# Optimization experiments

Hardware: AMD Instinct MI355X
Metric: run time of the kernel (lower is better)

## Reference

```python
import jax, jax.numpy as jnp
import numpy as np

N_LEAVES = 8192   # perfect binary tree, depth 13
SEQ = 4096        # sequenceSize
EMB = 100         # embedSize
NCLS = 2          # numClasses


def setup_inputs() -> dict:
    key = jax.random.key(0)
    k = jax.random.split(key, 7)
    return {
        "leaf_seqs": jax.random.normal(k[0], (N_LEAVES, SEQ), dtype=jnp.float32),
        # torch nn.Linear stores weight as [out, in]; y = x @ W.T + b
        "We": jax.random.normal(k[1], (EMB, SEQ), dtype=jnp.float32) / np.sqrt(SEQ).astype(np.float32),
        "be": jax.random.normal(k[2], (EMB,), dtype=jnp.float32) * 0.01,
        "W": jax.random.normal(k[3], (EMB, 2 * EMB), dtype=jnp.float32) / np.sqrt(2 * EMB).astype(np.float32),
        "b": jax.random.normal(k[4], (EMB,), dtype=jnp.float32) * 0.01,
        "Wp": jax.random.normal(k[5], (NCLS, EMB), dtype=jnp.float32) / np.sqrt(EMB).astype(np.float32),
        "bp": jax.random.normal(k[6], (NCLS,), dtype=jnp.float32) * 0.01,
    }


def reference(leaf_seqs, We, be, W, b, Wp, bp):
    # Level-order (tree-batched) evaluation of the recursive RNN over a
    # perfect binary tree. Leaves: relu(embedding(seq)); internal nodes:
    # relu(W @ cat(left, right)); root: projection -> class logits.
    h = jax.nn.relu(leaf_seqs @ We.T + be)              # [n_leaves, emb]
    depth = int(np.log2(N_LEAVES))
    for _ in range(depth):                               # fixed small loop over levels
        # adjacent siblings: reshape gives cat((left, right), dim=1) per pair
        pairs = h.reshape(h.shape[0] // 2, 2 * h.shape[1])  # [n/2, 2*emb]
        h = jax.nn.relu(pairs @ W.T + b)                 # [n/2, emb]
    logits = h @ Wp.T + bp                               # [1, numClasses]
    return logits
```

## Files before the change

### kernel.cpp

```cpp
#include <hip/hip_runtime.h>


typedef _Float16 half_t;
typedef __attribute__((ext_vector_type(8))) _Float16 half8;
typedef __attribute__((ext_vector_type(4))) float floatx4;

__global__ __launch_bounds__(256) void bprep(const float* __restrict__ We,
                                             half_t* __restrict__ Bf) {
  int t = blockIdx.x * 256 + threadIdx.x;
  int lane = t & 63;
  int c = (t >> 6) & 7;
  int ks = t >> 9;
  int q = lane >> 4, m = lane & 15;
  int n = c * 16 + m;
  int k0 = ks * 32 + q * 8;

  half8 hv, lv;
#pragma unroll
  for (int j = 0; j < 8; ++j) {
    float w = (n < 100) ? We[(size_t)n * 4096 + k0 + j] : 0.f;
    half_t hh = (half_t)w;
    hv[j] = hh;
    lv[j] = (half_t)(w - (float)hh);
  }
  size_t fhi = (size_t)(ks * 16 + c * 2 + 0) * 64 + lane;
  size_t flo = (size_t)(ks * 16 + c * 2 + 1) * 64 + lane;
  *(half8*)(Bf + fhi * 8) = hv;
  *(half8*)(Bf + flo * 8) = lv;
}

__global__ __launch_bounds__(512, 1) void leaf_mfma(const float* __restrict__ A,
                                                    const half8* __restrict__ Bf,
                                                    const float* __restrict__ be,
                                                    float* __restrict__ h0) {
  __shared__ float red[4 * 32 * 128];
  const int tid = threadIdx.x;
  const int lane = tid & 63;
  const int wave = tid >> 6;
  const int q = lane >> 4, m = lane & 15;
  const int r0 = blockIdx.x * 32;

  floatx4 acc[2][8];
#pragma unroll
  for (int t = 0; t < 2; ++t)
#pragma unroll
    for (int c = 0; c < 8; ++c) acc[t][c] = (floatx4){0.f, 0.f, 0.f, 0.f};

  const float* a0 = A + (size_t)(r0 + m) * 4096 + wave * 512 + q * 8;
  const float* a1 = a0 + (size_t)16 * 4096;
  const half8* bw = Bf + (size_t)wave * 256 * 64 + lane;

  floatx4 acur[4], anxt[4];
  acur[0] = *(const floatx4*)(a0);
  acur[1] = *(const floatx4*)(a0 + 4);
  acur[2] = *(const floatx4*)(a1);
  acur[3] = *(const floatx4*)(a1 + 4);

  for (int s = 0; s < 16; ++s) {
    if (s < 15) {
      const float* p0 = a0 + (s + 1) * 32;
      const float* p1 = a1 + (s + 1) * 32;
      anxt[0] = *(const floatx4*)(p0);
      anxt[1] = *(const floatx4*)(p0 + 4);
      anxt[2] = *(const floatx4*)(p1);
      anxt[3] = *(const floatx4*)(p1 + 4);
    }
    half8 ahi[2], alo[2];
#pragma unroll
    for (int t = 0; t < 2; ++t) {
#pragma unroll
      for (int j = 0; j < 8; ++j) {
        float v = acur[2 * t + (j >> 2)][j & 3];
        half_t hh = (half_t)v;
        ahi[t][j] = hh;
        alo[t][j] = (half_t)(v - (float)hh);
      }
    }
    const half8* bs = bw + s * 1024;
#pragma unroll
    for (int c = 0; c < 8; ++c) {
      half8 bhi = bs[c * 128];
      half8 blo = bs[c * 128 + 64];
      acc[0][c] = __builtin_amdgcn_mfma_f32_16x16x32_f16(ahi[0], bhi, acc[0][c], 0, 0, 0);
      acc[1][c] = __builtin_amdgcn_mfma_f32_16x16x32_f16(ahi[1], bhi, acc[1][c], 0, 0, 0);
      acc[0][c] = __builtin_amdgcn_mfma_f32_16x16x32_f16(alo[0], bhi, acc[0][c], 0, 0, 0);
      acc[1][c] = __builtin_amdgcn_mfma_f32_16x16x32_f16(alo[1], bhi, acc[1][c], 0, 0, 0);
      acc[0][c] = __builtin_amdgcn_mfma_f32_16x16x32_f16(ahi[0], blo, acc[0][c], 0, 0, 0);
      acc[1][c] = __builtin_amdgcn_mfma_f32_16x16x32_f16(ahi[1], blo, acc[1][c], 0, 0, 0);
    }
#pragma unroll
    for (int v = 0; v < 4; ++v) acur[v] = anxt[v];
  }

#pragma unroll
  for (int hstep = 4; hstep >= 1; hstep >>= 1) {
    if (wave >= hstep && wave < 2 * hstep) {
      float* d = red + (wave - hstep) * 4096;
#pragma unroll
      for (int t = 0; t < 2; ++t)
#pragma unroll
        for (int c = 0; c < 8; ++c)
#pragma unroll
          for (int r = 0; r < 4; ++r)
            d[(t * 16 + q * 4 + r) * 128 + c * 16 + m] = acc[t][c][r];
    }
    __syncthreads();
    if (wave < hstep) {
      const float* s2 = red + wave * 4096;
#pragma unroll
      for (int t = 0; t < 2; ++t)
#pragma unroll
        for (int c = 0; c < 8; ++c)
#pragma unroll
          for (int r = 0; r < 4; ++r)
            acc[t][c][r] += s2[(t * 16 + q * 4 + r) * 128 + c * 16 + m];
    }
    __syncthreads();
  }

  if (wave == 0) {
#pragma unroll
    for (int c = 0; c < 8; ++c) {
      int col = c * 16 + m;
      if (col < 100) {
        float bias = be[col];
#pragma unroll
        for (int t = 0; t < 2; ++t)
#pragma unroll
          for (int r = 0; r < 4; ++r) {
            int row = r0 + t * 16 + q * 4 + r;
            h0[(size_t)row * 100 + col] = fmaxf(acc[t][c][r] + bias, 0.f);
          }
      }
    }
  }
}

template <int NVEC>
__global__ __launch_bounds__(256, 1) void tree_stage(const float* __restrict__ in,
                                                     float* __restrict__ out,
                                                     const float* __restrict__ Wt,
                                                     const float* __restrict__ bt) {
  __shared__ __align__(16) float bufA[3200];
  __shared__ __align__(16) float bufB[1600];
  __shared__ __align__(16) float scr[1600];
  const int tid = threadIdx.x;
  const int j = tid & 127;
  const int s = tid >> 7;

  floatx4 Wf[25];
  if (j < 100) {
    const floatx4* wp = (const floatx4*)(Wt + j * 200 + s * 100);
#pragma unroll
    for (int qq = 0; qq < 25; ++qq) Wf[qq] = wp[qq];
  }
  const float* gin = in + (size_t)blockIdx.x * NVEC * 100;
  for (int t = tid; t < NVEC * 100; t += 256) bufA[t] = gin[t];
  float bj = (j < 100) ? bt[j] : 0.f;
  __syncthreads();

  float* src = bufA;
  float* dst = bufB;
  constexpr int LEVELS = (NVEC == 32) ? 5 : 3;
#pragma unroll
  for (int l = 0; l < LEVELS; ++l) {
    const int nout = NVEC >> (l + 1);
    float p[16];
    if (j < 100) {
#pragma unroll
      for (int n = 0; n < nout; ++n) {
        const floatx4* v = (const floatx4*)(src + n * 200 + s * 100);
        floatx4 a = (floatx4){0.f, 0.f, 0.f, 0.f};
#pragma unroll
        for (int qq = 0; qq < 25; ++qq) {
          floatx4 x = v[qq];
          a.x += Wf[qq].x * x.x; a.y += Wf[qq].y * x.y;
          a.z += Wf[qq].z * x.z; a.w += Wf[qq].w * x.w;
        }
        p[n] = (a.x + a.y) + (a.z + a.w);
      }
    }
    if (s == 1 && j < 100) {
#pragma unroll
      for (int n = 0; n < nout; ++n) scr[n * 100 + j] = p[n];
    }
    __syncthreads();
    if (s == 0 && j < 100) {
#pragma unroll
      for (int n = 0; n < nout; ++n)
        dst[n * 100 + j] = fmaxf(bj + p[n] + scr[n * 100 + j], 0.f);
    }
    __syncthreads();
    float* tmp = src; src = dst; dst = tmp;
  }
  if (tid < 100) out[(size_t)blockIdx.x * 100 + tid] = src[tid];
}

__global__ __launch_bounds__(256, 1) void tree_tail(const float* __restrict__ in,
                                                    const float* __restrict__ Wt,
                                                    const float* __restrict__ bt,
                                                    const float* __restrict__ Wp,
                                                    const float* __restrict__ bp,
                                                    float* __restrict__ logits) {
  __shared__ __align__(16) float bufA[800];
  __shared__ __align__(16) float bufB[400];
  __shared__ __align__(16) float scr[400];
  const int tid = threadIdx.x;
  const int j = tid & 127;
  const int s = tid >> 7;

  floatx4 Wf[25];
  if (j < 100) {
    const floatx4* wp = (const floatx4*)(Wt + j * 200 + s * 100);
#pragma unroll
    for (int qq = 0; qq < 25; ++qq) Wf[qq] = wp[qq];
  }
  for (int t = tid; t < 800; t += 256) bufA[t] = in[t];
  float bj = (j < 100) ? bt[j] : 0.f;
  __syncthreads();

  float* src = bufA;
  float* dst = bufB;
#pragma unroll
  for (int l = 0; l < 3; ++l) {
    const int nout = 8 >> (l + 1);
    float p[4];
    if (j < 100) {
#pragma unroll
      for (int n = 0; n < nout; ++n) {
        const floatx4* v = (const floatx4*)(src + n * 200 + s * 100);
        floatx4 a = (floatx4){0.f, 0.f, 0.f, 0.f};
#pragma unroll
        for (int qq = 0; qq < 25; ++qq) {
          floatx4 x = v[qq];
          a.x += Wf[qq].x * x.x; a.y += Wf[qq].y * x.y;
          a.z += Wf[qq].z * x.z; a.w += Wf[qq].w * x.w;
        }
        p[n] = (a.x + a.y) + (a.z + a.w);
      }
    }
    if (s == 1 && j < 100) {
#pragma unroll
      for (int n = 0; n < nout; ++n) scr[n * 100 + j] = p[n];
    }
    __syncthreads();
    if (s == 0 && j < 100) {
#pragma unroll
      for (int n = 0; n < nout; ++n)
        dst[n * 100 + j] = fmaxf(bj + p[n] + scr[n * 100 + j], 0.f);
    }
    __syncthreads();
    float* tmp = src; src = dst; dst = tmp;
  }
  if (tid < 128) {
    int cls = tid >> 6, l = tid & 63;
    float sum = Wp[cls * 100 + l] * src[l];
    if (l + 64 < 100) sum += Wp[cls * 100 + l + 64] * src[l + 64];
#pragma unroll
    for (int off = 32; off > 0; off >>= 1) sum += __shfl_down(sum, off, 64);
    if (l == 0) logits[cls] = sum + bp[cls];
  }
}

extern "C" void kernel_launch(void* const* d_in, const int* in_sizes, int n_in,
                              void* d_out, int out_size, void* d_ws, size_t ws_size,
                              hipStream_t stream) {
  (void)in_sizes; (void)n_in; (void)out_size; (void)ws_size;
  const float* leaf = (const float*)d_in[0];
  const float* We = (const float*)d_in[1];
  const float* be = (const float*)d_in[2];
  const float* W = (const float*)d_in[3];
  const float* b = (const float*)d_in[4];
  const float* Wp = (const float*)d_in[5];
  const float* bp = (const float*)d_in[6];
  float* out = (float*)d_out;

  char* ws = (char*)d_ws;
  half_t* Bf = (half_t*)ws;
  float* h0 = (float*)(ws + 2097152);
  float* h1 = h0 + 8192 * 100;
  float* h2 = h1 + 256 * 100;

  bprep<<<dim3(256), dim3(256), 0, stream>>>(We, Bf);
  leaf_mfma<<<dim3(256), dim3(512), 0, stream>>>(leaf, (const half8*)Bf, be, h0);
  tree_stage<32><<<dim3(256), dim3(256), 0, stream>>>(h0, h1, W, b);
  tree_stage<32><<<dim3(8), dim3(256), 0, stream>>>(h1, h2, W, b);
  tree_tail<<<dim3(1), dim3(256), 0, stream>>>(h2, W, b, Wp, bp, out);
}
```

Baseline: 284.7 us.

## Stage leaf tiles via LDS DMA, trim N padding, and move tree levels to MFMA

The leaf GEMM now streams A tiles into double-buffered LDS with global_load_lds, where before each wave loaded them directly into registers. It also drops the padded eighth 16-column tile, since 7 tiles cover 100 outputs. The tree levels switch from scalar FP32 dot products to split-fp16 MFMA, using a new prepacked W layout built by a wprep kernel. The tail becomes a generic tree_mfma call plus a small projection kernel. This adds an extra launch and syncthreads on every k-step, and the wave-per-k-slice split now uses a different k mapping.

```diff
diff --git a/kernel.cpp b/kernel.cpp
--- a/kernel.cpp
+++ b/kernel.cpp
@@ -5,131 +5,173 @@
 typedef __attribute__((ext_vector_type(8))) _Float16 half8;
 typedef __attribute__((ext_vector_type(4))) float floatx4;
 
+__device__ __forceinline__ void gld_lds16(const float* g, float* l) {
+  __builtin_amdgcn_global_load_lds((const __attribute__((address_space(1))) void*)g,
+                                   (__attribute__((address_space(3))) void*)l, 16, 0, 0);
+}
+
+__device__ __forceinline__ void cvt_hilo(const floatx4& a, const floatx4& b, half8& hi, half8& lo) {
+#pragma unroll
+  for (int j = 0; j < 4; ++j) {
+    float v = a[j];
+    half_t hh = (half_t)v;
+    hi[j] = hh; lo[j] = (half_t)(v - (float)hh);
+  }
+#pragma unroll
+  for (int j = 0; j < 4; ++j) {
+    float v = b[j];
+    half_t hh = (half_t)v;
+    hi[4 + j] = hh; lo[4 + j] = (half_t)(v - (float)hh);
+  }
+}
+
 __global__ __launch_bounds__(256) void bprep(const float* __restrict__ We,
                                              half_t* __restrict__ Bf) {
   int t = blockIdx.x * 256 + threadIdx.x;
-  int lane = t & 63;
-  int c = (t >> 6) & 7;
-  int ks = t >> 9;
-  int q = lane >> 4, m = lane & 15;
-  int n = c * 16 + m;
-  int k0 = ks * 32 + q * 8;
-
+  if (t >= 51200) return;
+  int n = t >> 9;
+  int kp = t & 511;
+  int k0 = kp * 8;
+  int ks = k0 >> 5;
+  int q = (k0 >> 3) & 3;
+  int c = n >> 4, m = n & 15;
+  int lane = q * 16 + m;
+
+  const float* src = We + (size_t)n * 4096 + k0;
   half8 hv, lv;
 #pragma unroll
   for (int j = 0; j < 8; ++j) {
-    float w = (n < 100) ? We[(size_t)n * 4096 + k0 + j] : 0.f;
+    float w = src[j];
     half_t hh = (half_t)w;
-    hv[j] = hh;
-    lv[j] = (half_t)(w - (float)hh);
-  }
-  size_t fhi = (size_t)(ks * 16 + c * 2 + 0) * 64 + lane;
-  size_t flo = (size_t)(ks * 16 + c * 2 + 1) * 64 + lane;
-  *(half8*)(Bf + fhi * 8) = hv;
-  *(half8*)(Bf + flo * 8) = lv;
+    hv[j] = hh; lv[j] = (half_t)(w - (float)hh);
+  }
+  size_t base = (size_t)(ks * 14 + c * 2) * 64 + lane;
+  *(half8*)(Bf + base * 8) = hv;
+  *(half8*)(Bf + (base + 64) * 8) = lv;
+}
+
+__global__ __launch_bounds__(64) void wprep(const float* __restrict__ W,
+                                            half_t* __restrict__ Wf) {
+  int ks = blockIdx.x / 7, tt = blockIdx.x % 7;
+  int lane = threadIdx.x;
+  int q = lane >> 4, n = lane & 15;
+  int col = tt * 16 + n;
+  int kb = ks * 32 + q * 8;
+  half8 hv, lv;
+#pragma unroll
+  for (int j = 0; j < 8; ++j) {
+    int k = kb + j;
+    float w = (col < 100 && k < 200) ? W[(size_t)col * 200 + k] : 0.f;
+    half_t hh = (half_t)w;
+    hv[j] = hh; lv[j] = (half_t)(w - (float)hh);
+  }
+  size_t base = (size_t)(ks * 14 + tt * 2) * 64 + lane;
+  *(half8*)(Wf + base * 8) = hv;
+  *(half8*)(Wf + (base + 64) * 8) = lv;
 }
 
 __global__ __launch_bounds__(512, 1) void leaf_mfma(const float* __restrict__ A,
                                                     const half8* __restrict__ Bf,
                                                     const float* __restrict__ be,
                                                     float* __restrict__ h0) {
-  __shared__ float red[4 * 32 * 128];
+  __shared__ __align__(16) float lds[2 * 32 * 260];
   const int tid = threadIdx.x;
   const int lane = tid & 63;
   const int wave = tid >> 6;
   const int q = lane >> 4, m = lane & 15;
   const int r0 = blockIdx.x * 32;
 
-  floatx4 acc[2][8];
+  floatx4 acc[2][7];
 #pragma unroll
   for (int t = 0; t < 2; ++t)
 #pragma unroll
-    for (int c = 0; c < 8; ++c) acc[t][c] = (floatx4){0.f, 0.f, 0.f, 0.f};
-
-  const float* a0 = A + (size_t)(r0 + m) * 4096 + wave * 512 + q * 8;
-  const float* a1 = a0 + (size_t)16 * 4096;
-  const half8* bw = Bf + (size_t)wave * 256 * 64 + lane;
-
-  floatx4 acur[4], anxt[4];
-  acur[0] = *(const floatx4*)(a0);
-  acur[1] = *(const floatx4*)(a0 + 4);
-  acur[2] = *(const floatx4*)(a1);
-  acur[3] = *(const floatx4*)(a1 + 4);
-
-  for (int s = 0; s < 16; ++s) {
-    if (s < 15) {
-      const float* p0 = a0 + (s + 1) * 32;
-      const float* p1 = a1 + (s + 1) * 32;
-      anxt[0] = *(const floatx4*)(p0);
-      anxt[1] = *(const floatx4*)(p0 + 4);
-      anxt[2] = *(const floatx4*)(p1);
-      anxt[3] = *(const floatx4*)(p1 + 4);
-    }
+    for (int c = 0; c < 7; ++c) acc[t][c] = (floatx4){0.f, 0.f, 0.f, 0.f};
+
+  {
+    const float* g = A + (size_t)(r0 + wave * 4) * 4096 + lane * 4;
+    float* d = lds + (wave * 4) * 260 + lane * 4;
+#pragma unroll
+    for (int i = 0; i < 4; ++i) gld_lds16(g + (size_t)i * 4096, d + i * 260);
+  }
+  __syncthreads();
+
+  for (int t = 0; t < 16; ++t) {
+    float* cur = lds + (t & 1) * 8320;
+    float* nxt = lds + ((t + 1) & 1) * 8320;
+
+    const int ksg = t * 8 + wave;
+    const half8* bb = Bf + (size_t)(ksg * 14) * 64 + lane;
+    half8 bhi[7], blo[7];
+#pragma unroll
+    for (int c = 0; c < 7; ++c) { bhi[c] = bb[c * 128]; blo[c] = bb[c * 128 + 64]; }
+
+    if (t < 15) {
+      const float* g = A + (size_t)(r0 + wave * 4) * 4096 + (t + 1) * 256 + lane * 4;
+      float* d = nxt + (wave * 4) * 260 + lane * 4;
+#pragma unroll
+      for (int i = 0; i < 4; ++i) gld_lds16(g + (size_t)i * 4096, d + i * 260);
+    }
+
+    const float* ap = cur + m * 260 + wave * 32 + q * 8;
+    floatx4 a0 = *(const floatx4*)ap;
+    floatx4 a1 = *(const floatx4*)(ap + 4);
+    floatx4 a2 = *(const floatx4*)(ap + 16 * 260);
+    floatx4 a3 = *(const floatx4*)(ap + 16 * 260 + 4);
     half8 ahi[2], alo[2];
-#pragma unroll
-    for (int t = 0; t < 2; ++t) {
-#pragma unroll
-      for (int j = 0; j < 8; ++j) {
-        float v = acur[2 * t + (j >> 2)][j & 3];
-        half_t hh = (half_t)v;
-        ahi[t][j] = hh;
-        alo[t][j] = (half_t)(v - (float)hh);
-      }
-    }
-    const half8* bs = bw + s * 1024;
-#pragma unroll
-    for (int c = 0; c < 8; ++c) {
-      half8 bhi = bs[c * 128];
-      half8 blo = bs[c * 128 + 64];
-      acc[0][c] = __builtin_amdgcn_mfma_f32_16x16x32_f16(ahi[0], bhi, acc[0][c], 0, 0, 0);
-      acc[1][c] = __builtin_amdgcn_mfma_f32_16x16x32_f16(ahi[1], bhi, acc[1][c], 0, 0, 0);
-      acc[0][c] = __builtin_amdgcn_mfma_f32_16x16x32_f16(alo[0], bhi, acc[0][c], 0, 0, 0);
-      acc[1][c] = __builtin_amdgcn_mfma_f32_16x16x32_f16(alo[1], bhi, acc[1][c], 0, 0, 0);
-      acc[0][c] = __builtin_amdgcn_mfma_f32_16x16x32_f16(ahi[0], blo, acc[0][c], 0, 0, 0);
-      acc[1][c] = __builtin_amdgcn_mfma_f32_16x16x32_f16(ahi[1], blo, acc[1][c], 0, 0, 0);
-    }
-#pragma unroll
-    for (int v = 0; v < 4; ++v) acur[v] = anxt[v];
-  }
-
-#pragma unroll
-  for (int hstep = 4; hstep >= 1; hstep >>= 1) {
-    if (wave >= hstep && wave < 2 * hstep) {
-      float* d = red + (wave - hstep) * 4096;
+    cvt_hilo(a0, a1, ahi[0], alo[0]);
+    cvt_hilo(a2, a3, ahi[1], alo[1]);
+
+#pragma unroll
+    for (int c = 0; c < 7; ++c) {
+      acc[0][c] = __builtin_amdgcn_mfma_f32_16x16x32_f16(ahi[0], bhi[c], acc[0][c], 0, 0, 0);
+      acc[1][c] = __builtin_amdgcn_mfma_f32_16x16x32_f16(ahi[1], bhi[c], acc[1][c], 0, 0, 0);
+      acc[0][c] = __builtin_amdgcn_mfma_f32_16x16x32_f16(alo[0], bhi[c], acc[0][c], 0, 0, 0);
+      acc[1][c] = __builtin_amdgcn_mfma_f32_16x16x32_f16(alo[1], bhi[c], acc[1][c], 0, 0, 0);
+      acc[0][c] = __builtin_amdgcn_mfma_f32_16x16x32_f16(ahi[0], blo[c], acc[0][c], 0, 0, 0);
+      acc[1][c] = __builtin_amdgcn_mfma_f32_16x16x32_f16(ahi[1], blo[c], acc[1][c], 0, 0, 0);
+    }
+    __syncthreads();
+  }
+
+  float* red = lds;
+#pragma unroll
+  for (int h = 4; h >= 1; h >>= 1) {
+    if (wave >= h && wave < 2 * h) {
+      float* d = red + (wave - h) * 3584;
 #pragma unroll
       for (int t = 0; t < 2; ++t)
 #pragma unroll
-        for (int c = 0; c < 8; ++c)
+        for (int c = 0; c < 7; ++c)
 #pragma unroll
           for (int r = 0; r < 4; ++r)
-            d[(t * 16 + q * 4 + r) * 128 + c * 16 + m] = acc[t][c][r];
-    }
-    __syncthreads();
-    if (wave < hstep) {
-      const float* s2 = red + wave * 4096;
+            d[(t * 16 + q * 4 + r) * 112 + c * 16 + m] = acc[t][c][r];
+    }
+    __syncthreads();
+    if (wave < h) {
+      const float* s = red + wave * 3584;
 #pragma unroll
       for (int t = 0; t < 2; ++t)
 #pragma unroll
-        for (int c = 0; c < 8; ++c)
+        for (int c = 0; c < 7; ++c)
 #pragma unroll
           for (int r = 0; r < 4; ++r)
-            acc[t][c][r] += s2[(t * 16 + q * 4 + r) * 128 + c * 16 + m];
+            acc[t][c][r] += s[(t * 16 + q * 4 + r) * 112 + c * 16 + m];
     }
     __syncthreads();
   }
 
   if (wave == 0) {
 #pragma unroll
-    for (int c = 0; c < 8; ++c) {
+    for (int c = 0; c < 7; ++c) {
       int col = c * 16 + m;
       if (col < 100) {
-        float bias = be[col];
+        float bv = be[col];
 #pragma unroll
         for (int t = 0; t < 2; ++t)
 #pragma unroll
           for (int r = 0; r < 4; ++r) {
             int row = r0 + t * 16 + q * 4 + r;
-            h0[(size_t)row * 100 + col] = fmaxf(acc[t][c][r] + bias, 0.f);
+            h0[(size_t)row * 100 + col] = fmaxf(acc[t][c][r] + bv, 0.f);
           }
       }
     }
@@ -137,129 +179,91 @@
 }
 
 template <int NVEC>
-__global__ __launch_bounds__(256, 1) void tree_stage(const float* __restrict__ in,
-                                                     float* __restrict__ out,
-                                                     const float* __restrict__ Wt,
-                                                     const float* __restrict__ bt) {
-  __shared__ __align__(16) float bufA[3200];
-  __shared__ __align__(16) float bufB[1600];
-  __shared__ __align__(16) float scr[1600];
+__global__ __launch_bounds__(256, 1) void tree_mfma(const float* __restrict__ in,
+                                                    float* __restrict__ out,
+                                                    const half8* __restrict__ Wf,
+                                                    const float* __restrict__ bt) {
+  __shared__ __align__(16) float bufA[16 * 228];
+  __shared__ __align__(16) float bufB[16 * 228];
   const int tid = threadIdx.x;
-  const int j = tid & 127;
-  const int s = tid >> 7;
-
-  floatx4 Wf[25];
-  if (j < 100) {
-    const floatx4* wp = (const floatx4*)(Wt + j * 200 + s * 100);
-#pragma unroll
-    for (int qq = 0; qq < 25; ++qq) Wf[qq] = wp[qq];
-  }
+  const int lane = tid & 63;
+  const int wave = tid >> 6;
+  const int q = lane >> 4, m = lane & 15;
+  const int t0 = 2 * wave;
+  const int t1 = (2 * wave + 1 > 6) ? 6 : 2 * wave + 1;
+
+  half8 wh0[7], wl0[7], wh1[7], wl1[7];
+#pragma unroll
+  for (int ks = 0; ks < 7; ++ks) {
+    wh0[ks] = Wf[(size_t)(ks * 14 + t0 * 2) * 64 + lane];
+    wl0[ks] = Wf[(size_t)(ks * 14 + t0 * 2 + 1) * 64 + lane];
+    wh1[ks] = Wf[(size_t)(ks * 14 + t1 * 2) * 64 + lane];
+    wl1[ks] = Wf[(size_t)(ks * 14 + t1 * 2 + 1) * 64 + lane];
+  }
+  const int c0 = t0 * 16 + m;
+  const int c1 = t1 * 16 + m;
+  const float b0 = (c0 < 100) ? bt[c0] : 0.f;
+  const float b1 = (c1 < 100) ? bt[c1] : 0.f;
+
+  for (int i = tid; i < 16 * 228; i += 256) { bufA[i] = 0.f; bufB[i] = 0.f; }
+  __syncthreads();
   const float* gin = in + (size_t)blockIdx.x * NVEC * 100;
-  for (int t = tid; t < NVEC * 100; t += 256) bufA[t] = gin[t];
-  float bj = (j < 100) ? bt[j] : 0.f;
+  for (int i = tid; i < NVEC * 100; i += 256) {
+    int v = i / 100, j = i - v * 100;
+    bufA[(v >> 1) * 228 + (v & 1) * 100 + j] = gin[i];
+  }
   __syncthreads();
 
   float* src = bufA;
   float* dst = bufB;
-  constexpr int LEVELS = (NVEC == 32) ? 5 : 3;
-#pragma unroll
-  for (int l = 0; l < LEVELS; ++l) {
+  constexpr int L = (NVEC == 32) ? 5 : 3;
+#pragma unroll
+  for (int l = 0; l < L; ++l) {
     const int nout = NVEC >> (l + 1);
-    float p[16];
-    if (j < 100) {
-#pragma unroll
-      for (int n = 0; n < nout; ++n) {
-        const floatx4* v = (const floatx4*)(src + n * 200 + s * 100);
-        floatx4 a = (floatx4){0.f, 0.f, 0.f, 0.f};
-#pragma unroll
-        for (int qq = 0; qq < 25; ++qq) {
-          floatx4 x = v[qq];
-          a.x += Wf[qq].x * x.x; a.y += Wf[qq].y * x.y;
-          a.z += Wf[qq].z * x.z; a.w += Wf[qq].w * x.w;
-        }
-        p[n] = (a.x + a.y) + (a.z + a.w);
+    floatx4 acc0 = (floatx4){0.f, 0.f, 0.f, 0.f};
+    floatx4 acc1 = (floatx4){0.f, 0.f, 0.f, 0.f};
+#pragma unroll
+    for (int ks = 0; ks < 7; ++ks) {
+      const float* ap = src + m * 228 + ks * 32 + q * 8;
+      floatx4 x0 = *(const floatx4*)ap;
+      floatx4 x1 = *(const floatx4*)(ap + 4);
+      half8 ah, al;
+      cvt_hilo(x0, x1, ah, al);
+      acc0 = __builtin_amdgcn_mfma_f32_16x16x32_f16(ah, wh0[ks], acc0, 0, 0, 0);
+      acc1 = __builtin_amdgcn_mfma_f32_16x16x32_f16(ah, wh1[ks], acc1, 0, 0, 0);
+      acc0 = __builtin_amdgcn_mfma_f32_16x16x32_f16(al, wh0[ks], acc0, 0, 0, 0);
+      acc1 = __builtin_amdgcn_mfma_f32_16x16x32_f16(al, wh1[ks], acc1, 0, 0, 0);
+      acc0 = __builtin_amdgcn_mfma_f32_16x16x32_f16(ah, wl0[ks], acc0, 0, 0, 0);
+      acc1 = __builtin_amdgcn_mfma_f32_16x16x32_f16(ah, wl1[ks], acc1, 0, 0, 0);
+    }
+#pragma unroll
+    for (int r = 0; r < 4; ++r) {
+      int rowR = q * 4 + r;
+      if (rowR < nout) {
+        if (c0 < 100)
+          dst[(rowR >> 1) * 228 + (rowR & 1) * 100 + c0] = fmaxf(acc0[r] + b0, 0.f);
+        if (t1 != t0 && c1 < 100)
+          dst[(rowR >> 1) * 228 + (rowR & 1) * 100 + c1] = fmaxf(acc1[r] + b1, 0.f);
       }
     }
-    if (s == 1 && j < 100) {
-#pragma unroll
-      for (int n = 0; n < nout; ++n) scr[n * 100 + j] = p[n];
-    }
-    __syncthreads();
-    if (s == 0 && j < 100) {
-#pragma unroll
-      for (int n = 0; n < nout; ++n)
-        dst[n * 100 + j] = fmaxf(bj + p[n] + scr[n * 100 + j], 0.f);
-    }
     __syncthreads();
     float* tmp = src; src = dst; dst = tmp;
   }
   if (tid < 100) out[(size_t)blockIdx.x * 100 + tid] = src[tid];
 }
 
-__global__ __launch_bounds__(256, 1) void tree_tail(const float* __restrict__ in,
-                                                    const float* __restrict__ Wt,
-                                                    const float* __restrict__ bt,
-                                                    const float* __restrict__ Wp,
-                                                    const float* __restrict__ bp,
-                                                    float* __restrict__ logits) {
-  __shared__ __align__(16) float bufA[800];
-  __shared__ __align__(16) float bufB[400];
-  __shared__ __align__(16) float scr[400];
+__global__ __launch_bounds__(128) void proj_kernel(const float* __restrict__ h,
+                                                   const float* __restrict__ Wp,
+                                                   const float* __restrict__ bp,
+                                                   float* __restrict__ out) {
   const int tid = threadIdx.x;
-  const int j = tid & 127;
-  const int s = tid >> 7;
-
-  floatx4 Wf[25];
-  if (j < 100) {
-    const floatx4* wp = (const floatx4*)(Wt + j * 200 + s * 100);
-#pragma unroll
-    for (int qq = 0; qq < 25; ++qq) Wf[qq] = wp[qq];
-  }
-  for (int t = tid; t < 800; t += 256) bufA[t] = in[t];
-  float bj = (j < 100) ? bt[j] : 0.f;
-  __syncthreads();
-
-  float* src = bufA;
-  float* dst = bufB;
-#pragma unroll
-  for (int l = 0; l < 3; ++l) {
-    const int nout = 8 >> (l + 1);
-    float p[4];
-    if (j < 100) {
-#pragma unroll
-      for (int n = 0; n < nout; ++n) {
-        const floatx4* v = (const floatx4*)(src + n * 200 + s * 100);
-        floatx4 a = (floatx4){0.f, 0.f, 0.f, 0.f};
-#pragma unroll
-        for (int qq = 0; qq < 25; ++qq) {
-          floatx4 x = v[qq];
-          a.x += Wf[qq].x * x.x; a.y += Wf[qq].y * x.y;
-          a.z += Wf[qq].z * x.z; a.w += Wf[qq].w * x.w;
-        }
-        p[n] = (a.x + a.y) + (a.z + a.w);
-      }
-    }
-    if (s == 1 && j < 100) {
-#pragma unroll
-      for (int n = 0; n < nout; ++n) scr[n * 100 + j] = p[n];
-    }
-    __syncthreads();
-    if (s == 0 && j < 100) {
-#pragma unroll
-      for (int n = 0; n < nout; ++n)
-        dst[n * 100 + j] = fmaxf(bj + p[n] + scr[n * 100 + j], 0.f);
-    }
-    __syncthreads();
-    float* tmp = src; src = dst; dst = tmp;
-  }
-  if (tid < 128) {
-    int cls = tid >> 6, l = tid & 63;
-    float sum = Wp[cls * 100 + l] * src[l];
-    if (l + 64 < 100) sum += Wp[cls * 100 + l + 64] * src[l + 64];
-#pragma unroll
-    for (int off = 32; off > 0; off >>= 1) sum += __shfl_down(sum, off, 64);
-    if (l == 0) logits[cls] = sum + bp[cls];
-  }
+  const int cls = tid >> 6;
+  const int l = tid & 63;
+  float sum = Wp[cls * 100 + l] * h[l];
+  if (l + 64 < 100) sum += Wp[cls * 100 + l + 64] * h[l + 64];
+#pragma unroll
+  for (int off = 32; off > 0; off >>= 1) sum += __shfl_down(sum, off, 64);
+  if (l == 0) out[cls] = sum + bp[cls];
 }
 
 extern "C" void kernel_launch(void* const* d_in, const int* in_sizes, int n_in,
@@ -277,13 +281,17 @@
 
   char* ws = (char*)d_ws;
   half_t* Bf = (half_t*)ws;
-  float* h0 = (float*)(ws + 2097152);
-  float* h1 = h0 + 8192 * 100;
-  float* h2 = h1 + 256 * 100;
-
-  bprep<<<dim3(256), dim3(256), 0, stream>>>(We, Bf);
+  half_t* Wfr = (half_t*)(ws + 1835008);
+  float* h0 = (float*)(ws + 1935360);
+  float* h1 = (float*)(ws + 5212160);
+  float* h2 = (float*)(ws + 5314560);
+  float* h3 = (float*)(ws + 5317760);
+
+  bprep<<<dim3(200), dim3(256), 0, stream>>>(We, Bf);
+  wprep<<<dim3(49), dim3(64), 0, stream>>>(W, Wfr);
   leaf_mfma<<<dim3(256), dim3(512), 0, stream>>>(leaf, (const half8*)Bf, be, h0);
-  tree_stage<32><<<dim3(256), dim3(256), 0, stream>>>(h0, h1, W, b);
-  tree_stage<32><<<dim3(8), dim3(256), 0, stream>>>(h1, h2, W, b);
-  tree_tail<<<dim3(1), dim3(256), 0, stream>>>(h2, W, b, Wp, bp, out);
-}
+  tree_mfma<32><<<dim3(256), dim3(256), 0, stream>>>(h0, h1, (const half8*)Wfr, b);
+  tree_mfma<32><<<dim3(8), dim3(256), 0, stream>>>(h1, h2, (const half8*)Wfr, b);
+  tree_mfma<8><<<dim3(1), dim3(256), 0, stream>>>(h2, h3, (const half8*)Wfr, b);
+  proj_kernel<<<dim3(1), dim3(128), 0, stream>>>(h3, Wp, bp, out);
+}
```

Measured after the change: 256.0 us. -10.1%, faster.
